# Performance work log

Measured on AMD Instinct MI355X. Metric: run time of the kernel, lower is better.

Reference implementation:

```python
import jax, jax.numpy as jnp
import numpy as np

BATCH = 2048
NUM_FIELDS = 32
EMBED = 64
NPAIRS = NUM_FIELDS * (NUM_FIELDS - 1) // 2  # 496
# static pair indices (i < j), same order as the torch double loop
ROW, COL = np.triu_indices(NUM_FIELDS, k=1)
ROW = jnp.asarray(ROW)
COL = jnp.asarray(COL)


def setup_inputs() -> dict:
    key = jax.random.key(0)
    k1, k2 = jax.random.split(key)
    emb_inputs = jax.random.normal(k1, (BATCH, NUM_FIELDS, EMBED), dtype=jnp.float32)
    # xavier_normal_ on kernel of shape (E, NC2, E): fan_in = NC2*E (dims[1:]), fan_out = E*E... 
    # torch: fan_in = size(1)*receptive = NPAIRS*EMBED? torch uses size(1)*prod(size[2:]) = NPAIRS*EMBED,
    # fan_out = size(0)*prod(size[2:]) = EMBED*EMBED; std = sqrt(2/(fan_in+fan_out))
    fan_in = NPAIRS * EMBED
    fan_out = EMBED * EMBED
    std = float(np.sqrt(2.0 / (fan_in + fan_out)))
    kernel = jax.random.normal(k2, (EMBED, NPAIRS, EMBED), dtype=jnp.float32) * std
    return {"emb_inputs": emb_inputs, "kernel": kernel}


def reference(emb_inputs, kernel):
    # emb_inputs: (B, N, E); kernel: (E, NC2, E)
    p = emb_inputs[:, ROW]  # (B, NC2, E)
    q = emb_inputs[:, COL]  # (B, NC2, E)
    # torch: kp[b,i,pair] = sum_j p[b,pair,j] * kernel[i,pair,j]; out[b,pair] = sum_i kp*q
    kp = jnp.einsum('bpj,ipj->bpi', p, kernel)  # (B, NC2, E) -- avoids (B,E,NC2,E) blowup
    outputs = jnp.sum(kp * q, axis=-1)          # (B, NC2)
    return outputs[:, None, :]                  # (B, 1, NC2)
```

## Files before the change

### kernel.cpp

```cpp
#include <hip/hip_runtime.h>
#include <hip/hip_bf16.h>

#define BATCH   2048
#define NFIELDS 32
#define EMBED   64
#define NPAIRS  496
#define BT      256
#define NIT     4
#define TPB     16
#define NBT     (BATCH / BT)
#define PPX     62

typedef __attribute__((ext_vector_type(8))) short bf16x8;
typedef __attribute__((ext_vector_type(4))) float f32x4;

__device__ __forceinline__ unsigned short f2bf(float x) {
    unsigned int u = __float_as_uint(x);
    unsigned int r = 0x7fffu + ((u >> 16) & 1u);
    return (unsigned short)((u + r) >> 16);
}

#define PP_OFF 0
#define PQ_OFF 4194304
#define KB_OFF 8388608
#define WS_ELEMS 10420224

__global__ __launch_bounds__(256) void prepass(
    const float* __restrict__ emb, const float* __restrict__ kern,
    unsigned short* __restrict__ ws)
{
    unsigned short* pp = ws + PP_OFF;
    unsigned short* pq = ws + PQ_OFF;
    unsigned short* kb = ws + KB_OFF;
    const int NEMB8 = BATCH * NFIELDS * EMBED / 8;
    const int NKER8 = EMBED * NPAIRS * EMBED / 8;
    int v = blockIdx.x * blockDim.x + threadIdx.x;
    if (v < NEMB8) {
        int base = v * 8;
        int e0 = base & 63;
        int f  = (base >> 6) & 31;
        int b  = base >> 11;
        float4 v0 = *(const float4*)(emb + base);
        float4 v1 = *(const float4*)(emb + base + 4);
        ushort4 lo, hi;
        lo.x = f2bf(v0.x); lo.y = f2bf(v0.y); lo.z = f2bf(v0.z); lo.w = f2bf(v0.w);
        hi.x = f2bf(v1.x); hi.y = f2bf(v1.y); hi.z = f2bf(v1.z); hi.w = f2bf(v1.w);
        int t = b >> 4, col = b & 15;
        int ks = e0 >> 5, quad = (e0 & 31) >> 3;
        size_t dp = (size_t)f * 131072 + t * 1024 + ks * 512 + quad * 128 + col * 8;
        *(ushort4*)(pp + dp)     = lo;
        *(ushort4*)(pp + dp + 4) = hi;
        int pos  = e0 & 31;
        int half = pos >> 4;
        int qq   = (pos & 15) >> 2;
        size_t dq = (size_t)f * 131072 + t * 1024 + ks * 512 + qq * 128 + col * 8 + half * 4;
        *(ushort4*)(pq + dq)       = lo;
        *(ushort4*)(pq + dq + 128) = hi;
    } else if (v < NEMB8 + NKER8) {
        int base = (v - NEMB8) * 8;
        int j0 = base & 63;
        int pr = (base >> 6) % NPAIRS;
        int i  = (base >> 6) / NPAIRS;
        float4 v0 = *(const float4*)(kern + base);
        float4 v1 = *(const float4*)(kern + base + 4);
        ushort4 lo, hi;
        lo.x = f2bf(v0.x); lo.y = f2bf(v0.y); lo.z = f2bf(v0.z); lo.w = f2bf(v0.w);
        hi.x = f2bf(v1.x); hi.y = f2bf(v1.y); hi.z = f2bf(v1.z); hi.w = f2bf(v1.w);
        size_t dk = (size_t)pr * 4096 + i * 64 + j0;
        *(ushort4*)(kb + dk)     = lo;
        *(ushort4*)(kb + dk + 4) = hi;
    }
}

__global__ __launch_bounds__(256) void opn_main(
    const unsigned short* __restrict__ ws, float* __restrict__ out)
{
    const unsigned short* pp = ws + PP_OFF;
    const unsigned short* pq = ws + PQ_OFF;
    const unsigned short* kb = ws + KB_OFF;

    const int bx   = blockIdx.x;
    const int slot = bx >> 3;
    const int pair = (bx & 7) * PPX + slot % PPX;
    const int bt   = slot / PPX;

    int r = 0, s0 = 0;
    while (pair >= s0 + (NFIELDS - 1 - r)) { s0 += NFIELDS - 1 - r; ++r; }
    const int c = r + 1 + (pair - s0);

    const int tid = threadIdx.x;
    const int wave = tid >> 6, lane = tid & 63;
    const int col = lane & 15, quad = lane >> 4;

    bf16x8 kfr[4][2];
    const unsigned short* kp = kb + (size_t)pair * 4096;
    #pragma unroll
    for (int mt = 0; mt < 4; ++mt)
        #pragma unroll
        for (int ks = 0; ks < 2; ++ks)
            kfr[mt][ks] = *(const bf16x8*)(kp + (mt*16 + col)*64 + ks*32 + quad*8);

    const int T0 = bt * TPB + wave * NIT;
    const unsigned short* pbase = pp + (size_t)r * 131072 + (size_t)T0 * 1024 + lane * 8;
    const unsigned short* qbase = pq + (size_t)c * 131072 + (size_t)T0 * 1024 + lane * 8;

    bf16x8 pA[NIT], pB[NIT];
    uint4  qA[NIT], qB[NIT];
    #pragma unroll
    for (int it = 0; it < NIT; ++it) {
        pA[it] = *(const bf16x8*)(pbase + it*1024);
        pB[it] = *(const bf16x8*)(pbase + it*1024 + 512);
        qA[it] = *(const uint4*)(qbase + it*1024);
        qB[it] = *(const uint4*)(qbase + it*1024 + 512);
    }

    #pragma unroll
    for (int it = 0; it < NIT; ++it) {
        f32x4 acc[4];
        #pragma unroll
        for (int mt = 0; mt < 4; ++mt) {
            acc[mt] = (f32x4){0.f, 0.f, 0.f, 0.f};
            acc[mt] = __builtin_amdgcn_mfma_f32_16x16x32_bf16(kfr[mt][0], pA[it], acc[mt], 0, 0, 0);
            acc[mt] = __builtin_amdgcn_mfma_f32_16x16x32_bf16(kfr[mt][1], pB[it], acc[mt], 0, 0, 0);
        }

        float partial = 0.f;
        {
            uint4 qa = qA[it], qb = qB[it];
            partial += acc[0][0] * __uint_as_float(qa.x << 16);
            partial += acc[0][1] * __uint_as_float(qa.x & 0xffff0000u);
            partial += acc[0][2] * __uint_as_float(qa.y << 16);
            partial += acc[0][3] * __uint_as_float(qa.y & 0xffff0000u);
            partial += acc[1][0] * __uint_as_float(qa.z << 16);
            partial += acc[1][1] * __uint_as_float(qa.z & 0xffff0000u);
            partial += acc[1][2] * __uint_as_float(qa.w << 16);
            partial += acc[1][3] * __uint_as_float(qa.w & 0xffff0000u);
            partial += acc[2][0] * __uint_as_float(qb.x << 16);
            partial += acc[2][1] * __uint_as_float(qb.x & 0xffff0000u);
            partial += acc[2][2] * __uint_as_float(qb.y << 16);
            partial += acc[2][3] * __uint_as_float(qb.y & 0xffff0000u);
            partial += acc[3][0] * __uint_as_float(qb.z << 16);
            partial += acc[3][1] * __uint_as_float(qb.z & 0xffff0000u);
            partial += acc[3][2] * __uint_as_float(qb.w << 16);
            partial += acc[3][3] * __uint_as_float(qb.w & 0xffff0000u);
        }
        partial += __shfl_xor(partial, 16, 64);
        partial += __shfl_xor(partial, 32, 64);

        if (quad == 0)
            out[(size_t)((T0 + it) * 16 + col) * NPAIRS + pair] = partial;
    }
}

__global__ __launch_bounds__(256) void opn_naive(
    const float* __restrict__ emb, const float* __restrict__ kern,
    float* __restrict__ out)
{
    int idx = blockIdx.x * blockDim.x + threadIdx.x;
    if (idx >= BATCH * NPAIRS) return;
    int b = idx / NPAIRS, p = idx % NPAIRS;
    int r = 0, s0 = 0;
    while (p >= s0 + (NFIELDS - 1 - r)) { s0 += NFIELDS - 1 - r; ++r; }
    int c = r + 1 + (p - s0);
    const float* pv = emb + ((size_t)b * NFIELDS + r) * EMBED;
    const float* qv = emb + ((size_t)b * NFIELDS + c) * EMBED;
    float acc = 0.f;
    for (int i = 0; i < EMBED; ++i) {
        const float* kr = kern + ((size_t)i * NPAIRS + p) * EMBED;
        float kpv = 0.f;
        for (int j = 0; j < EMBED; ++j) kpv += kr[j] * pv[j];
        acc += kpv * qv[i];
    }
    out[(size_t)b * NPAIRS + p] = acc;
}

extern "C" void kernel_launch(void* const* d_in, const int* in_sizes, int n_in,
                              void* d_out, int out_size, void* d_ws, size_t ws_size,
                              hipStream_t stream) {
    const float* emb  = (const float*)d_in[0];
    const float* kern = (const float*)d_in[1];
    float* out = (float*)d_out;

    if (ws_size >= (size_t)WS_ELEMS * sizeof(unsigned short)) {
        unsigned short* ws = (unsigned short*)d_ws;
        const int NEMB8 = BATCH * NFIELDS * EMBED / 8;
        const int NKER8 = EMBED * NPAIRS * EMBED / 8;
        int total = NEMB8 + NKER8;
        prepass<<<(total + 255) / 256, 256, 0, stream>>>(emb, kern, ws);
        opn_main<<<dim3(NPAIRS * NBT), 256, 0, stream>>>(ws, out);
    } else {
        int total = BATCH * NPAIRS;
        opn_naive<<<(total + 255) / 256, 256, 0, stream>>>(emb, kern, out);
    }
}
```

Before: 109.9 us.

## Drop separate Q layout, write pair-major output, add transpose kernel

Removes the second bf16 copy of the embeddings (pq) and instead reads the q values for the elementwise product from the shared pp layout with per-lane uint2 gathers. Work is remapped so each wave handles a different pair and each block covers 128 batch rows in two chunks. Output is written pair-major into a workspace buffer, which gives contiguous stores, and then a new LDS-tiled transpose kernel converts it to batch-major. This cuts prepass write traffic and strided output stores, at the cost of an extra kernel launch, an extra output round trip and narrower q loads.

```diff
diff --git a/kernel.cpp b/kernel.cpp
--- a/kernel.cpp
+++ b/kernel.cpp
@@ -5,11 +5,11 @@
 #define NFIELDS 32
 #define EMBED   64
 #define NPAIRS  496
-#define BT      256
+#define BT      128
 #define NIT     4
-#define TPB     16
+#define NCH     2
 #define NBT     (BATCH / BT)
-#define PPX     62
+#define NPG     (NPAIRS / 4)
 
 typedef __attribute__((ext_vector_type(8))) short bf16x8;
 typedef __attribute__((ext_vector_type(4))) float f32x4;
@@ -21,16 +21,15 @@
 }
 
 #define PP_OFF 0
-#define PQ_OFF 4194304
-#define KB_OFF 8388608
-#define WS_ELEMS 10420224
+#define KB_OFF 4194304
+#define OT_OFF_BYTES 12451840
+#define WS_BYTES (OT_OFF_BYTES + 2048*496*4)
 
 __global__ __launch_bounds__(256) void prepass(
     const float* __restrict__ emb, const float* __restrict__ kern,
     unsigned short* __restrict__ ws)
 {
     unsigned short* pp = ws + PP_OFF;
-    unsigned short* pq = ws + PQ_OFF;
     unsigned short* kb = ws + KB_OFF;
     const int NEMB8 = BATCH * NFIELDS * EMBED / 8;
     const int NKER8 = EMBED * NPAIRS * EMBED / 8;
@@ -50,12 +49,6 @@
         size_t dp = (size_t)f * 131072 + t * 1024 + ks * 512 + quad * 128 + col * 8;
         *(ushort4*)(pp + dp)     = lo;
         *(ushort4*)(pp + dp + 4) = hi;
-        int pos  = e0 & 31;
-        int half = pos >> 4;
-        int qq   = (pos & 15) >> 2;
-        size_t dq = (size_t)f * 131072 + t * 1024 + ks * 512 + qq * 128 + col * 8 + half * 4;
-        *(ushort4*)(pq + dq)       = lo;
-        *(ushort4*)(pq + dq + 128) = hi;
     } else if (v < NEMB8 + NKER8) {
         int base = (v - NEMB8) * 8;
         int j0 = base & 63;
@@ -73,24 +66,23 @@
 }
 
 __global__ __launch_bounds__(256) void opn_main(
-    const unsigned short* __restrict__ ws, float* __restrict__ out)
+    const unsigned short* __restrict__ ws, float* __restrict__ outT)
 {
     const unsigned short* pp = ws + PP_OFF;
-    const unsigned short* pq = ws + PQ_OFF;
     const unsigned short* kb = ws + KB_OFF;
 
-    const int bx   = blockIdx.x;
-    const int slot = bx >> 3;
-    const int pair = (bx & 7) * PPX + slot % PPX;
-    const int bt   = slot / PPX;
-
+    const int bx = blockIdx.x;
+    const int t  = bx & 15;
+    const int g  = bx >> 4;
+
+    const int tid = threadIdx.x;
+    const int wave = tid >> 6, lane = tid & 63;
+    const int col = lane & 15, quad = lane >> 4;
+
+    const int pair = g * 4 + wave;
     int r = 0, s0 = 0;
     while (pair >= s0 + (NFIELDS - 1 - r)) { s0 += NFIELDS - 1 - r; ++r; }
     const int c = r + 1 + (pair - s0);
-
-    const int tid = threadIdx.x;
-    const int wave = tid >> 6, lane = tid & 63;
-    const int col = lane & 15, quad = lane >> 4;
 
     bf16x8 kfr[4][2];
     const unsigned short* kp = kb + (size_t)pair * 4096;
@@ -100,55 +92,76 @@
         for (int ks = 0; ks < 2; ++ks)
             kfr[mt][ks] = *(const bf16x8*)(kp + (mt*16 + col)*64 + ks*32 + quad*8);
 
-    const int T0 = bt * TPB + wave * NIT;
-    const unsigned short* pbase = pp + (size_t)r * 131072 + (size_t)T0 * 1024 + lane * 8;
-    const unsigned short* qbase = pq + (size_t)c * 131072 + (size_t)T0 * 1024 + lane * 8;
-
-    bf16x8 pA[NIT], pB[NIT];
-    uint4  qA[NIT], qB[NIT];
-    #pragma unroll
-    for (int it = 0; it < NIT; ++it) {
-        pA[it] = *(const bf16x8*)(pbase + it*1024);
-        pB[it] = *(const bf16x8*)(pbase + it*1024 + 512);
-        qA[it] = *(const uint4*)(qbase + it*1024);
-        qB[it] = *(const uint4*)(qbase + it*1024 + 512);
-    }
-
-    #pragma unroll
-    for (int it = 0; it < NIT; ++it) {
-        f32x4 acc[4];
+    const unsigned short* pfield = pp + (size_t)r * 131072;
+    const unsigned short* qfield = pp + (size_t)c * 131072;
+    const int qlaneoff = (quad >> 1) * 128 + col * 8 + (quad & 1) * 4;
+
+    float* otp = outT + (size_t)pair * BATCH;
+
+    #pragma unroll
+    for (int s = 0; s < NCH; ++s) {
+        const int T0 = t * (BT/16) + s * NIT;
+
+        bf16x8 pA[NIT], pB[NIT];
+        uint2  qv[NIT][4];
         #pragma unroll
-        for (int mt = 0; mt < 4; ++mt) {
-            acc[mt] = (f32x4){0.f, 0.f, 0.f, 0.f};
-            acc[mt] = __builtin_amdgcn_mfma_f32_16x16x32_bf16(kfr[mt][0], pA[it], acc[mt], 0, 0, 0);
-            acc[mt] = __builtin_amdgcn_mfma_f32_16x16x32_bf16(kfr[mt][1], pB[it], acc[mt], 0, 0, 0);
+        for (int it = 0; it < NIT; ++it) {
+            const unsigned short* pt = pfield + (size_t)(T0 + it) * 1024;
+            const unsigned short* qt = qfield + (size_t)(T0 + it) * 1024;
+            pA[it] = *(const bf16x8*)(pt + lane * 8);
+            pB[it] = *(const bf16x8*)(pt + 512 + lane * 8);
+            #pragma unroll
+            for (int mt = 0; mt < 4; ++mt)
+                qv[it][mt] = *(const uint2*)(qt + (mt >> 1) * 512 + (mt & 1) * 256 + qlaneoff);
         }
 
-        float partial = 0.f;
-        {
-            uint4 qa = qA[it], qb = qB[it];
-            partial += acc[0][0] * __uint_as_float(qa.x << 16);
-            partial += acc[0][1] * __uint_as_float(qa.x & 0xffff0000u);
-            partial += acc[0][2] * __uint_as_float(qa.y << 16);
-            partial += acc[0][3] * __uint_as_float(qa.y & 0xffff0000u);
-            partial += acc[1][0] * __uint_as_float(qa.z << 16);
-            partial += acc[1][1] * __uint_as_float(qa.z & 0xffff0000u);
-            partial += acc[1][2] * __uint_as_float(qa.w << 16);
-            partial += acc[1][3] * __uint_as_float(qa.w & 0xffff0000u);
-            partial += acc[2][0] * __uint_as_float(qb.x << 16);
-            partial += acc[2][1] * __uint_as_float(qb.x & 0xffff0000u);
-            partial += acc[2][2] * __uint_as_float(qb.y << 16);
-            partial += acc[2][3] * __uint_as_float(qb.y & 0xffff0000u);
-            partial += acc[3][0] * __uint_as_float(qb.z << 16);
-            partial += acc[3][1] * __uint_as_float(qb.z & 0xffff0000u);
-            partial += acc[3][2] * __uint_as_float(qb.w << 16);
-            partial += acc[3][3] * __uint_as_float(qb.w & 0xffff0000u);
+        #pragma unroll
+        for (int it = 0; it < NIT; ++it) {
+            f32x4 acc[4];
+            #pragma unroll
+            for (int mt = 0; mt < 4; ++mt) {
+                acc[mt] = (f32x4){0.f, 0.f, 0.f, 0.f};
+                acc[mt] = __builtin_amdgcn_mfma_f32_16x16x32_bf16(kfr[mt][0], pA[it], acc[mt], 0, 0, 0);
+                acc[mt] = __builtin_amdgcn_mfma_f32_16x16x32_bf16(kfr[mt][1], pB[it], acc[mt], 0, 0, 0);
+            }
+
+            float partial = 0.f;
+            #pragma unroll
+            for (int mt = 0; mt < 4; ++mt) {
+                uint2 qd = qv[it][mt];
+                partial += acc[mt][0] * __uint_as_float(qd.x << 16);
+                partial += acc[mt][1] * __uint_as_float(qd.x & 0xffff0000u);
+                partial += acc[mt][2] * __uint_as_float(qd.y << 16);
+                partial += acc[mt][3] * __uint_as_float(qd.y & 0xffff0000u);
+            }
+            partial += __shfl_xor(partial, 16, 64);
+            partial += __shfl_xor(partial, 32, 64);
+
+            if (quad == 0)
+                otp[(T0 + it) * 16 + col] = partial;
         }
-        partial += __shfl_xor(partial, 16, 64);
-        partial += __shfl_xor(partial, 32, 64);
-
-        if (quad == 0)
-            out[(size_t)((T0 + it) * 16 + col) * NPAIRS + pair] = partial;
+    }
+}
+
+__global__ __launch_bounds__(256) void transpose_out(
+    const float* __restrict__ outT, float* __restrict__ out)
+{
+    __shared__ float tile[32][33];
+    const int p0 = blockIdx.x * 32;
+    const int b0 = blockIdx.y * 32;
+    const int tx = threadIdx.x & 31, ty = threadIdx.x >> 5;
+    #pragma unroll
+    for (int k = 0; k < 4; ++k) {
+        int p = p0 + ty + k * 8;
+        if (p < NPAIRS)
+            tile[ty + k * 8][tx] = outT[(size_t)p * BATCH + b0 + tx];
+    }
+    __syncthreads();
+    #pragma unroll
+    for (int k = 0; k < 4; ++k) {
+        int b = b0 + ty + k * 8;
+        if (p0 + tx < NPAIRS)
+            out[(size_t)b * NPAIRS + p0 + tx] = tile[tx][ty + k * 8];
     }
 }
 
@@ -181,13 +194,15 @@
     const float* kern = (const float*)d_in[1];
     float* out = (float*)d_out;
 
-    if (ws_size >= (size_t)WS_ELEMS * sizeof(unsigned short)) {
+    if (ws_size >= (size_t)WS_BYTES) {
         unsigned short* ws = (unsigned short*)d_ws;
+        float* outT = (float*)((char*)d_ws + OT_OFF_BYTES);
         const int NEMB8 = BATCH * NFIELDS * EMBED / 8;
         const int NKER8 = EMBED * NPAIRS * EMBED / 8;
         int total = NEMB8 + NKER8;
         prepass<<<(total + 255) / 256, 256, 0, stream>>>(emb, kern, ws);
-        opn_main<<<dim3(NPAIRS * NBT), 256, 0, stream>>>(ws, out);
+        opn_main<<<dim3(NPG * NBT), 256, 0, stream>>>(ws, outT);
+        transpose_out<<<dim3(16, 64), 256, 0, stream>>>(outT, out);
     } else {
         int total = BATCH * NPAIRS;
         opn_naive<<<(total + 255) / 256, 256, 0, stream>>>(emb, kern, out);
```

After: 107.4 us. 1.02x faster.
